# Performance work log

Measured on AMD Instinct MI355X. Metric: run time of the kernel, lower is better.

The kernel has to match this reference:

```python
import jax, jax.numpy as jnp
import numpy as np

T, B, H, W, C = 256, 1024, 9, 9, 3
CTX, HID, ACT = 64, 256, 7

def setup_inputs() -> dict:
    key = jax.random.key(0)
    ks = jax.random.split(key, 16)
    s = 0.05
    return {
        'image': jax.random.normal(ks[0], (T, B, H, W, C), jnp.float32),
        'agent_dir': jax.random.randint(ks[1], (T, B), 0, 4, jnp.int32),
        'dones': jax.random.bernoulli(ks[2], 0.02, (T, B)),
        'context': jax.random.normal(ks[3], (B, CTX), jnp.float32),
        'c0': jnp.zeros((B, HID), jnp.float32),
        'h0': jnp.zeros((B, HID), jnp.float32),
        'conv_k': jax.random.normal(ks[4], (3, 3, C, 16), jnp.float32) * s,
        'conv_b': jnp.zeros((16,), jnp.float32),
        'emb_k': jax.random.normal(ks[5], (4, 5), jnp.float32) * s,
        'emb_b': jnp.zeros((5,), jnp.float32),
        'wi': jax.random.normal(ks[6], (784 + 5 + CTX, 4 * HID), jnp.float32) * s,
        'wh': jax.random.normal(ks[7], (HID, 4 * HID), jnp.float32) * s,
        'b_lstm': jnp.zeros((4 * HID,), jnp.float32),
        'a0_k': jax.random.normal(ks[8], (HID, 32), jnp.float32) * s,
        'a0_b': jnp.zeros((32,), jnp.float32),
        'a1_k': jax.random.normal(ks[9], (32, ACT), jnp.float32) * s,
        'a1_b': jnp.zeros((ACT,), jnp.float32),
        'cr0_k': jax.random.normal(ks[10], (HID, 32), jnp.float32) * s,
        'cr0_b': jnp.zeros((32,), jnp.float32),
        'cr1_k': jax.random.normal(ks[11], (32, 1), jnp.float32) * s,
        'cr1_b': jnp.zeros((1,), jnp.float32),
    }


def reference(image, agent_dir, dones, context, c0, h0, conv_k, conv_b,
              emb_k, emb_b, wi, wh, b_lstm, a0_k, a0_b, a1_k, a1_b,
              cr0_k, cr0_b, cr1_k, cr1_b):
    t, b = image.shape[:2]
    # Conv(16, 3x3, VALID) over flattened (T*B) batch, NHWC
    x = image.reshape(t * b, *image.shape[2:])
    img = jax.lax.conv_general_dilated(
        x, conv_k, window_strides=(1, 1), padding='VALID',
        dimension_numbers=('NHWC', 'HWIO', 'NHWC')) + conv_b
    img = jax.nn.relu(img.reshape(t, b, -1))  # (T, B, 784)
    # direction embedding: one_hot(4) -> Dense(5)
    dir_e = jax.nn.one_hot(agent_dir, 4, dtype=img.dtype) @ emb_k + emb_b
    # context broadcast over time
    ctx = jnp.broadcast_to(context[None], (t, b, context.shape[-1]))
    emb = jnp.concatenate([img, dir_e, ctx], axis=-1)  # (T, B, 853)
    # precompute input-side LSTM gates (big batched GEMM outside the scan)
    xg = emb @ wi + b_lstm  # (T, B, 4*HID)

    def step(carry, inp):
        c, h = carry
        xg_t, done = inp
        mask = done[:, None]
        c = jnp.where(mask, c0, c)  # reset carry at episode boundaries
        h = jnp.where(mask, h0, h)
        gates = xg_t + h @ wh
        i, f, g, o = jnp.split(gates, 4, axis=-1)  # flax order: i, f, g, o
        new_c = jax.nn.sigmoid(f) * c + jax.nn.sigmoid(i) * jnp.tanh(g)
        new_h = jax.nn.sigmoid(o) * jnp.tanh(new_c)
        return (new_c, new_h), new_h

    (c_fin, h_fin), ys = jax.lax.scan(step, (c0, h0), (xg, dones))
    actor = jax.nn.relu(ys @ a0_k + a0_b)
    logits = actor @ a1_k + a1_b  # Categorical logits
    critic = jax.nn.relu(ys @ cr0_k + cr0_b)
    value = jnp.squeeze(critic @ cr1_k + cr1_b, axis=-1)
    return c_fin, h_fin, logits, value
```

## Files before the change

kernel.cpp:

```cpp
#include <hip/hip_runtime.h>
#include <hip/hip_fp8.h>

typedef __bf16 bf16;
typedef __bf16 bf16x8 __attribute__((ext_vector_type(8)));
typedef __bf16 bf16x4 __attribute__((ext_vector_type(4)));
typedef float  f32x4  __attribute__((ext_vector_type(4)));

#define T_DIM 256
#define B_DIM 1024
#define HID   256
#define G4    1024
#define KIMG  784
#define KPAD  800
#define KEXT  864
#define CTXD  64
#define MROWS (T_DIM*B_DIM)
#define WPITCH 264

__device__ __forceinline__ void gll16(const void* g, void* l) {
  __builtin_amdgcn_global_load_lds((const __attribute__((address_space(1))) void*)g,
                                   (__attribute__((address_space(3))) void*)l, 16, 0, 0);
}
__device__ __forceinline__ float sigm(float x) { return 1.f / (1.f + __expf(-x)); }
__device__ __forceinline__ float tanh_(float x) {
  x = fminf(fmaxf(x, -15.f), 15.f);
  float e = __expf(2.f * x);
  return (e - 1.f) / (e + 1.f);
}
__device__ __forceinline__ void bar_lds() {
  asm volatile("s_waitcnt lgkmcnt(0)\n\ts_barrier" ::: "memory");
}
__device__ __forceinline__ unsigned char to_fp8(float f) {
  __hip_fp8_e4m3 v(f);
  return *reinterpret_cast<unsigned char*>(&v);
}

__global__ void k_wiT(const float* __restrict__ wi, bf16* __restrict__ wiT) {
  int n = blockIdx.x;
  for (int k = threadIdx.x; k < KEXT; k += 256) {
    float v = 0.f;
    if (k < KIMG) v = wi[(long)k * G4 + n];
    else if (k >= 800) v = wi[(long)(k - 11) * G4 + n];
    wiT[(long)n * KEXT + k] = (bf16)v;
  }
}
__global__ void k_ext(const float* __restrict__ ctx, bf16* __restrict__ ext) {
  int idx = blockIdx.x * 256 + threadIdx.x;
  ext[idx] = (bf16)ctx[idx];
}
__global__ void k_wh8(const float* __restrict__ wh, unsigned char* __restrict__ wh8) {
  int n = blockIdx.x;
  int k = threadIdx.x;
#pragma unroll
  for (int g = 0; g < 4; ++g)
    wh8[g * 65536 + n * 256 + k] = to_fp8(wh[k * G4 + g * 256 + n]);
}
__global__ void k_W0T(const float* __restrict__ a0k, const float* __restrict__ cr0k,
                      bf16* __restrict__ w0t) {
  int n = blockIdx.x;
  int k = threadIdx.x;
  float v = (n < 32) ? a0k[k * 32 + n] : cr0k[k * 32 + (n - 32)];
  w0t[n * HID + k] = (bf16)v;
}
__global__ void k_dirgate(const float* __restrict__ wi, const float* __restrict__ emb_k,
                          const float* __restrict__ emb_b, const float* __restrict__ b_lstm,
                          float* __restrict__ dir_gate) {
  int d = blockIdx.x;
  for (int n = threadIdx.x; n < G4; n += 256) {
    float s = b_lstm[n];
#pragma unroll
    for (int j = 0; j < 5; ++j) s += (emb_k[d * 5 + j] + emb_b[j]) * wi[(KIMG + j) * G4 + n];
    dir_gate[d * G4 + n] = s;
  }
}

#define CONV_ROWS 8
__global__ void k_conv(const float* __restrict__ img, const float* __restrict__ ck,
                       const float* __restrict__ cb, bf16* __restrict__ out) {
  __shared__ float s_img[CONV_ROWS * 243];
  __shared__ float s_k[432];
  __shared__ float s_b[16];
  long r0 = (long)blockIdx.x * CONV_ROWS;
  const float* src = img + r0 * 243;
  for (int i = threadIdx.x; i < CONV_ROWS * 243; i += 256) s_img[i] = src[i];
  for (int i = threadIdx.x; i < 432; i += 256) s_k[i] = ck[i];
  if (threadIdx.x < 16) s_b[threadIdx.x] = cb[threadIdx.x];
  __syncthreads();
  for (int idx = threadIdx.x; idx < CONV_ROWS * KPAD; idx += 256) {
    int r = idx / KPAD, c = idx % KPAD;
    float v = 0.f;
    if (c < KIMG) {
      int pix = c >> 4, ch = c & 15;
      int oy = pix / 7, ox = pix % 7;
      const float* ib = s_img + r * 243 + (oy * 9 + ox) * 3;
      v = s_b[ch];
#pragma unroll
      for (int ky = 0; ky < 3; ++ky)
#pragma unroll
        for (int kx = 0; kx < 3; ++kx)
#pragma unroll
          for (int cc = 0; cc < 3; ++cc)
            v += ib[(ky * 9 + kx) * 3 + cc] * s_k[((ky * 3 + kx) * 3 + cc) * 16 + ch];
      v = fmaxf(v, 0.f);
    }
    out[r0 * KPAD + idx] = (bf16)v;
  }
}

__global__ __launch_bounds__(256, 2)
void k_gemm_xg(const bf16* __restrict__ A, const bf16* __restrict__ ext,
               const bf16* __restrict__ Bt, const float* __restrict__ dir_gate,
               const int* __restrict__ agent_dir, bf16* __restrict__ xg) {
  __shared__ __align__(16) bf16 As[128 * 32];
  __shared__ __align__(16) bf16 Bs[128 * 32];
  const int bid = blockIdx.x;
  const int xcd = bid & 7, local = bid >> 3;
  const long m0 = (long)(xcd * 256 + (local >> 3)) * 128;
  const int n0 = (local & 7) * 128;
  const int tid = threadIdx.x, wave = tid >> 6, lane = tid & 63;
  const int row16 = lane & 15, k8 = (lane >> 4) * 8, rowg = (lane >> 4) * 4;
  const int wr = (wave >> 1) * 64, wc = (wave & 1) * 64;

  const bf16* a_src0 = A + (m0 + tid / 4) * KPAD + (tid % 4) * 8;
  const bf16* a_src1 = A + (m0 + 64 + tid / 4) * KPAD + (tid % 4) * 8;
  const bf16* e_src0 = ext + (long)(((m0) & 1023) + tid / 4) * CTXD + (tid % 4) * 8;
  const bf16* e_src1 = ext + (long)(((m0 + 64) & 1023) + tid / 4) * CTXD + (tid % 4) * 8;
  const bf16* b_src0 = Bt + (long)(n0 + tid / 4) * KEXT + (tid % 4) * 8;
  const bf16* b_src1 = Bt + (long)(n0 + 64 + tid / 4) * KEXT + (tid % 4) * 8;
  bf16* asd0 = As + wave * 512;
  bf16* asd1 = As + 2048 + wave * 512;
  bf16* bsd0 = Bs + wave * 512;
  bf16* bsd1 = Bs + 2048 + wave * 512;

  f32x4 acc[4][4];
  const f32x4 zero = {0.f, 0.f, 0.f, 0.f};
#pragma unroll
  for (int i = 0; i < 4; ++i)
#pragma unroll
    for (int j = 0; j < 4; ++j) acc[i][j] = zero;

  for (int ks = 0; ks < 27; ++ks) {
    if (ks < 25) {
      const int ko = ks * 32;
      gll16(a_src0 + ko, asd0);
      gll16(a_src1 + ko, asd1);
    } else {
      const int ko = (ks - 25) * 32;
      gll16(e_src0 + ko, asd0);
      gll16(e_src1 + ko, asd1);
    }
    const int kb = ks * 32;
    gll16(b_src0 + kb, bsd0);
    gll16(b_src1 + kb, bsd1);
    __syncthreads();
    bf16x8 af[4], bfr[4];
#pragma unroll
    for (int i = 0; i < 4; ++i)
      af[i] = *(const bf16x8*)(As + (wr + 16 * i + row16) * 32 + k8);
#pragma unroll
    for (int j = 0; j < 4; ++j)
      bfr[j] = *(const bf16x8*)(Bs + (wc + 16 * j + row16) * 32 + k8);
#pragma unroll
    for (int i = 0; i < 4; ++i)
#pragma unroll
      for (int j = 0; j < 4; ++j)
        acc[i][j] = __builtin_amdgcn_mfma_f32_16x16x32_bf16(af[i], bfr[j], acc[i][j], 0, 0, 0);
    __syncthreads();
  }
#pragma unroll
  for (int i = 0; i < 4; ++i)
#pragma unroll
    for (int j = 0; j < 4; ++j)
#pragma unroll
      for (int r = 0; r < 4; ++r) {
        long row = m0 + wr + 16 * i + rowg + r;
        int colj = n0 + wc + 16 * j + row16;
        int dv = agent_dir[row];
        float base = dir_gate[dv * G4 + colj];
        int u = colj & 255, g = colj >> 8;
        xg[row * G4 + u * 4 + g] = (bf16)(acc[i][j][r] + base);
      }
}

__global__ __launch_bounds__(1024)
void k_lstm(const bf16* __restrict__ xg, const unsigned char* __restrict__ wh8,
            const int* __restrict__ dones,
            const float* __restrict__ c0, const float* __restrict__ h0,
            bf16* __restrict__ ys, float* __restrict__ cfin, float* __restrict__ hfin) {
  __shared__ __align__(16) unsigned char wi8_lds[256 * WPITCH];
  __shared__ __align__(16) unsigned char wg8_lds[256 * WPITCH];
  __shared__ __align__(16) unsigned char h8_lds[2][16 * WPITCH];
  const int tid = threadIdx.x;
  const int w = tid >> 6, lane = tid & 63;
  const int col = lane & 15;
  const int kq = lane >> 4;
  const int k8 = kq * 8;
  const int rowg = kq * 4;
  const int b0 = blockIdx.x * 16;
  const int ju = 16 * w + col;

  for (int i = tid; i < 256 * 32; i += 1024) {
    int row = i >> 5, c = i & 31;
    *(long long*)(wi8_lds + row * WPITCH + c * 8) =
        *(const long long*)(wh8 + row * 256 + c * 8);
    *(long long*)(wg8_lds + row * WPITCH + c * 8) =
        *(const long long*)(wh8 + 2 * 65536 + row * 256 + c * 8);
  }
  for (int i = tid; i < 16 * HID; i += 1024) {
    int m = i >> 8, j = i & 255;
    h8_lds[0][m * WPITCH + j] = to_fp8(h0[(b0 + m) * HID + j]);
  }

  float creg[4], c0reg[4];
  unsigned char h0b8[4];
#pragma unroll
  for (int r = 0; r < 4; ++r) {
    float v = c0[(b0 + rowg + r) * HID + ju];
    creg[r] = v; c0reg[r] = v;
    h0b8[r] = to_fp8(h0[(b0 + rowg + r) * HID + ju]);
  }
  const unsigned char* wfp = wh8 + 1 * 65536 + ju * 256 + k8;
  const unsigned char* wop = wh8 + 3 * 65536 + ju * 256 + k8;

  int4 dnA = *(const int4*)(dones + b0 + rowg);
  bf16x4 xc[4];
  {
    const bf16* xb = xg + (long)(b0 + rowg) * G4 + ju * 4;
#pragma unroll
    for (int r = 0; r < 4; ++r)
      xc[r] = *(const bf16x4*)(xb + (long)r * G4);
  }
  long long bfr[4], bor[4];
#pragma unroll
  for (int c = 0; c < 3; ++c) {
    bfr[c] = *(const long long*)(wfp + c * 32);
    bor[c] = *(const long long*)(wop + c * 32);
  }
  __syncthreads();

  const unsigned char* hr = h8_lds[0];
  unsigned char* hw = (unsigned char*)h8_lds[1];

#pragma unroll 1
  for (int t = 0; t < T_DIM; ++t) {
    const int tn = (t + 1 < T_DIM) ? t + 1 : (T_DIM - 1);
    f32x4 acc[4];
    const f32x4 zero = {0.f, 0.f, 0.f, 0.f};
#pragma unroll
    for (int g = 0; g < 4; ++g) acc[g] = zero;

    int4 dnB;
#pragma unroll
    for (int ks = 0; ks < 8; ++ks) {
      {
        const int kn = (ks + 3) & 7, slot = (ks + 3) & 3;
        bfr[slot] = *(const long long*)(wfp + kn * 32);
        bor[slot] = *(const long long*)(wop + kn * 32);
      }
      long long a8 = *(const long long*)(hr + col * WPITCH + ks * 32 + k8);
      long long bi8 = *(const long long*)(wi8_lds + ju * WPITCH + ks * 32 + k8);
      long long bg8 = *(const long long*)(wg8_lds + ju * WPITCH + ks * 32 + k8);
      __builtin_amdgcn_s_setprio(1);
      acc[0] = __builtin_amdgcn_mfma_f32_16x16x32_fp8_fp8(a8, bi8, acc[0], 0, 0, 0);
      acc[1] = __builtin_amdgcn_mfma_f32_16x16x32_fp8_fp8(a8, bfr[ks & 3], acc[1], 0, 0, 0);
      acc[2] = __builtin_amdgcn_mfma_f32_16x16x32_fp8_fp8(a8, bg8, acc[2], 0, 0, 0);
      acc[3] = __builtin_amdgcn_mfma_f32_16x16x32_fp8_fp8(a8, bor[ks & 3], acc[3], 0, 0, 0);
      __builtin_amdgcn_s_setprio(0);
      if (ks == 2)
        dnB = *(const int4*)(dones + (long)tn * B_DIM + b0 + rowg);
    }

    int dc[4] = {dnA.x, dnA.y, dnA.z, dnA.w};
    int dx[4] = {dnB.x, dnB.y, dnB.z, dnB.w};
#pragma unroll
    for (int r = 0; r < 4; ++r) {
      float c_old = dc[r] ? c0reg[r] : creg[r];
      float gi = acc[0][r] + (float)xc[r][0];
      float gf = acc[1][r] + (float)xc[r][1];
      float gg = acc[2][r] + (float)xc[r][2];
      float go = acc[3][r] + (float)xc[r][3];
      float cn = sigm(gf) * c_old + sigm(gi) * tanh_(gg);
      float hn = sigm(go) * tanh_(cn);
      creg[r] = cn;
      int m = rowg + r;
      ys[((long)t * B_DIM + b0 + m) * HID + ju] = (bf16)hn;
      hw[m * WPITCH + ju] = dx[r] ? h0b8[r] : to_fp8(hn);
      if (t == T_DIM - 1) {
        cfin[(b0 + m) * HID + ju] = cn;
        hfin[(b0 + m) * HID + ju] = hn;
      }
    }
    {
      const bf16* xb = xg + (long)(tn * B_DIM + b0 + rowg) * G4 + ju * 4;
#pragma unroll
      for (int r = 0; r < 4; ++r)
        xc[r] = *(const bf16x4*)(xb + (long)r * G4);
    }
    dnA = dnB;
    bar_lds();
    { const unsigned char* tmp = hr; hr = hw; hw = (unsigned char*)tmp; }
  }
}

#define H1PITCH 66
__global__ __launch_bounds__(256, 2)
void k_heads(const bf16* __restrict__ ys, const bf16* __restrict__ w0t,
             const float* __restrict__ a0b, const float* __restrict__ cr0b,
             const float* __restrict__ a1k, const float* __restrict__ a1b,
             const float* __restrict__ cr1k, const float* __restrict__ cr1b,
             float* __restrict__ logits, float* __restrict__ value) {
  __shared__ __align__(16) bf16 As[128 * 32];
  __shared__ __align__(16) bf16 Ws[64 * 264];
  __shared__ bf16 h1_lds[128 * H1PITCH];
  __shared__ float w2[32 * 8];
  const int tid = threadIdx.x, wave = tid >> 6, lane = tid & 63;
  const int row16 = lane & 15, k8 = (lane >> 4) * 8, rowg = (lane >> 4) * 4;
  const long m0 = (long)blockIdx.x * 128;
  for (int i = tid; i < 64 * 256; i += 256) {
    int n = i >> 8, k = i & 255;
    Ws[n * 264 + k] = w0t[i];
  }
  if (tid < 224) { int k = tid / 7, c = tid % 7; w2[k * 8 + c] = a1k[tid]; }
  else if (tid < 256) { int k = tid - 224; w2[k * 8 + 7] = cr1k[k]; }
  const bf16* a_src0 = ys + (m0 + tid / 4) * HID + (tid % 4) * 8;
  const bf16* a_src1 = ys + (m0 + 64 + tid / 4) * HID + (tid % 4) * 8;
  bf16* asd0 = As + wave * 512;
  bf16* asd1 = As + 2048 + wave * 512;
  f32x4 acc[2][4];
  const f32x4 zero = {0.f, 0.f, 0.f, 0.f};
#pragma unroll
  for (int i = 0; i < 2; ++i)
#pragma unroll
    for (int j = 0; j < 4; ++j) acc[i][j] = zero;
  for (int ks = 0; ks < 8; ++ks) {
    gll16(a_src0 + ks * 32, asd0);
    gll16(a_src1 + ks * 32, asd1);
    __syncthreads();
    bf16x8 bw[4];
#pragma unroll
    for (int j = 0; j < 4; ++j)
      bw[j] = *(const bf16x8*)(Ws + (16 * j + row16) * 264 + ks * 32 + k8);
#pragma unroll
    for (int i = 0; i < 2; ++i) {
      bf16x8 a = *(const bf16x8*)(As + (32 * wave + 16 * i + row16) * 32 + k8);
#pragma unroll
      for (int j = 0; j < 4; ++j)
        acc[i][j] = __builtin_amdgcn_mfma_f32_16x16x32_bf16(a, bw[j], acc[i][j], 0, 0, 0);
    }
    __syncthreads();
  }
#pragma unroll
  for (int i = 0; i < 2; ++i)
#pragma unroll
    for (int j = 0; j < 4; ++j)
#pragma unroll
      for (int r = 0; r < 4; ++r) {
        int rl = 32 * wave + 16 * i + rowg + r;
        int n = 16 * j + row16;
        float bias = (n < 32) ? a0b[n] : cr0b[n - 32];
        h1_lds[rl * H1PITCH + n] = (bf16)fmaxf(acc[i][j][r] + bias, 0.f);
      }
  __syncthreads();
  if (tid < 128) {
    const bf16* hp = h1_lds + tid * H1PITCH;
    float acc7[7];
#pragma unroll
    for (int c = 0; c < 7; ++c) acc7[c] = a1b[c];
    float accv = cr1b[0];
#pragma unroll 4
    for (int k = 0; k < 32; ++k) {
      float av = (float)hp[k];
      float cv = (float)hp[32 + k];
#pragma unroll
      for (int c = 0; c < 7; ++c) acc7[c] += av * w2[k * 8 + c];
      accv += cv * w2[k * 8 + 7];
    }
    long row = m0 + tid;
#pragma unroll
    for (int c = 0; c < 7; ++c) logits[row * 7 + c] = acc7[c];
    value[row] = accv;
  }
}

extern "C" void kernel_launch(void* const* d_in, const int* in_sizes, int n_in,
                              void* d_out, int out_size, void* d_ws, size_t ws_size,
                              hipStream_t stream) {
  const float* image = (const float*)d_in[0];
  const int* agent_dir = (const int*)d_in[1];
  const int* dones = (const int*)d_in[2];
  const float* context = (const float*)d_in[3];
  const float* c0 = (const float*)d_in[4];
  const float* h0 = (const float*)d_in[5];
  const float* conv_k = (const float*)d_in[6];
  const float* conv_b = (const float*)d_in[7];
  const float* emb_k = (const float*)d_in[8];
  const float* emb_b = (const float*)d_in[9];
  const float* wi = (const float*)d_in[10];
  const float* wh = (const float*)d_in[11];
  const float* b_lstm = (const float*)d_in[12];
  const float* a0_k = (const float*)d_in[13];
  const float* a0_b = (const float*)d_in[14];
  const float* a1_k = (const float*)d_in[15];
  const float* a1_b = (const float*)d_in[16];
  const float* cr0_k = (const float*)d_in[17];
  const float* cr0_b = (const float*)d_in[18];
  const float* cr1_k = (const float*)d_in[19];
  const float* cr1_b = (const float*)d_in[20];

  char* ws = (char*)d_ws;
  const size_t off_conv = 0;
  const size_t off_xg   = 419430400ULL;
  const size_t off_wiT  = off_xg  + 536870912ULL;
  const size_t off_W0T  = off_wiT + 1769472ULL;
  const size_t off_dirg = off_W0T + 32768ULL;
  const size_t off_wh8  = off_dirg + 16384ULL;
  const size_t off_ext  = off_wh8 + 262144ULL;
  const size_t total    = off_ext + 131072ULL;
  if (ws_size < total) return;

  bf16* conv_out = (bf16*)(ws + off_conv);
  bf16* xg       = (bf16*)(ws + off_xg);
  bf16* wiT      = (bf16*)(ws + off_wiT);
  bf16* W0T      = (bf16*)(ws + off_W0T);
  float* dir_gate = (float*)(ws + off_dirg);
  unsigned char* wh8 = (unsigned char*)(ws + off_wh8);
  bf16* ext = (bf16*)(ws + off_ext);
  bf16* ys = (bf16*)(ws + 0);

  float* out_cfin = (float*)d_out;
  float* out_hfin = out_cfin + 262144;
  float* out_logits = out_cfin + 524288;
  float* out_value = out_cfin + 524288 + 1835008;

  k_wiT<<<1024, 256, 0, stream>>>(wi, wiT);
  k_ext<<<256, 256, 0, stream>>>(context, ext);
  k_W0T<<<64, 256, 0, stream>>>(a0_k, cr0_k, W0T);
  k_dirgate<<<4, 256, 0, stream>>>(wi, emb_k, emb_b, b_lstm, dir_gate);
  k_wh8<<<256, 256, 0, stream>>>(wh, wh8);
  k_conv<<<MROWS / CONV_ROWS, 256, 0, stream>>>(image, conv_k, conv_b, conv_out);
  k_gemm_xg<<<16384, 256, 0, stream>>>(conv_out, ext, wiT, dir_gate, agent_dir, xg);
  k_lstm<<<64, 1024, 0, stream>>>(xg, wh8, dones, c0, h0, ys, out_cfin, out_hfin);
  k_heads<<<2048, 256, 0, stream>>>(ys, W0T, a0_b, cr0_b, a1_k, a1_b, cr1_k, cr1_b,
                                    out_logits, out_value);
}
```

Measured before the change: 2.381 ms.

## Widen xg GEMM K-tile to 64 with XOR-swizzled LDS and reordered K layout

The input-gate GEMM now stages 64-wide K slices per iteration instead of 32, halving the number of barrier-separated loop iterations (14 vs 27). The transposed weight matrix is re-laid out so the context block comes first in K (padded to 896), letting the first iteration load context and the rest load conv features. LDS reads use an XOR swizzle to avoid bank conflicts at the wider row pitch. This doubles LDS use per block, which may affect occupancy, and slightly enlarges the padded K range.

```diff
diff --git a/kernel.cpp b/kernel.cpp
--- a/kernel.cpp
+++ b/kernel.cpp
@@ -12,7 +12,7 @@
 #define G4    1024
 #define KIMG  784
 #define KPAD  800
-#define KEXT  864
+#define KB64  896
 #define CTXD  64
 #define MROWS (T_DIM*B_DIM)
 #define WPITCH 264
@@ -37,11 +37,11 @@
 
 __global__ void k_wiT(const float* __restrict__ wi, bf16* __restrict__ wiT) {
   int n = blockIdx.x;
-  for (int k = threadIdx.x; k < KEXT; k += 256) {
+  for (int k = threadIdx.x; k < KB64; k += 256) {
     float v = 0.f;
-    if (k < KIMG) v = wi[(long)k * G4 + n];
-    else if (k >= 800) v = wi[(long)(k - 11) * G4 + n];
-    wiT[(long)n * KEXT + k] = (bf16)v;
+    if (k < 64) v = wi[(long)(789 + k) * G4 + n];
+    else if (k < 848) v = wi[(long)(k - 64) * G4 + n];
+    wiT[(long)n * KB64 + k] = (bf16)v;
   }
 }
 __global__ void k_ext(const float* __restrict__ ctx, bf16* __restrict__ ext) {
@@ -111,26 +111,23 @@
 void k_gemm_xg(const bf16* __restrict__ A, const bf16* __restrict__ ext,
                const bf16* __restrict__ Bt, const float* __restrict__ dir_gate,
                const int* __restrict__ agent_dir, bf16* __restrict__ xg) {
-  __shared__ __align__(16) bf16 As[128 * 32];
-  __shared__ __align__(16) bf16 Bs[128 * 32];
+  __shared__ __align__(16) bf16 As[128 * 64];
+  __shared__ __align__(16) bf16 Bs[128 * 64];
   const int bid = blockIdx.x;
   const int xcd = bid & 7, local = bid >> 3;
   const long m0 = (long)(xcd * 256 + (local >> 3)) * 128;
   const int n0 = (local & 7) * 128;
   const int tid = threadIdx.x, wave = tid >> 6, lane = tid & 63;
-  const int row16 = lane & 15, k8 = (lane >> 4) * 8, rowg = (lane >> 4) * 4;
+  const int row16 = lane & 15, kq = lane >> 4, rowg = kq * 4;
   const int wr = (wave >> 1) * 64, wc = (wave & 1) * 64;
 
-  const bf16* a_src0 = A + (m0 + tid / 4) * KPAD + (tid % 4) * 8;
-  const bf16* a_src1 = A + (m0 + 64 + tid / 4) * KPAD + (tid % 4) * 8;
-  const bf16* e_src0 = ext + (long)(((m0) & 1023) + tid / 4) * CTXD + (tid % 4) * 8;
-  const bf16* e_src1 = ext + (long)(((m0 + 64) & 1023) + tid / 4) * CTXD + (tid % 4) * 8;
-  const bf16* b_src0 = Bt + (long)(n0 + tid / 4) * KEXT + (tid % 4) * 8;
-  const bf16* b_src1 = Bt + (long)(n0 + 64 + tid / 4) * KEXT + (tid % 4) * 8;
-  bf16* asd0 = As + wave * 512;
-  bf16* asd1 = As + 2048 + wave * 512;
-  bf16* bsd0 = Bs + wave * 512;
-  bf16* bsd1 = Bs + 2048 + wave * 512;
+  const int srow = 8 * wave + (lane >> 3);
+  const int csrc8 = ((lane & 7) ^ (lane >> 3)) * 8;
+  const bf16* a_base = A + (long)(m0 + srow) * KPAD + csrc8;
+  const bf16* e_base = ext + (long)((m0 & 1023) + srow) * CTXD + csrc8;
+  const bf16* b_base = Bt + (long)(n0 + srow) * KB64 + csrc8;
+  bf16* asd = As + wave * 512;
+  bf16* bsd = Bs + wave * 512;
 
   f32x4 acc[4][4];
   const f32x4 zero = {0.f, 0.f, 0.f, 0.f};
@@ -139,32 +136,38 @@
 #pragma unroll
     for (int j = 0; j < 4; ++j) acc[i][j] = zero;
 
-  for (int ks = 0; ks < 27; ++ks) {
-    if (ks < 25) {
-      const int ko = ks * 32;
-      gll16(a_src0 + ko, asd0);
-      gll16(a_src1 + ko, asd1);
+  const int swz = row16 & 7;
+  for (int ks = 0; ks < 14; ++ks) {
+    if (ks == 0) {
+#pragma unroll
+      for (int c = 0; c < 4; ++c) gll16(e_base + c * (32 * CTXD), asd + c * 2048);
     } else {
-      const int ko = (ks - 25) * 32;
-      gll16(e_src0 + ko, asd0);
-      gll16(e_src1 + ko, asd1);
-    }
-    const int kb = ks * 32;
-    gll16(b_src0 + kb, bsd0);
-    gll16(b_src1 + kb, bsd1);
+      const long ko = (long)(ks - 1) * 64;
+#pragma unroll
+      for (int c = 0; c < 4; ++c) gll16(a_base + c * (32 * KPAD) + ko, asd + c * 2048);
+    }
+    {
+      const long kb = (long)ks * 64;
+#pragma unroll
+      for (int c = 0; c < 4; ++c) gll16(b_base + c * (32 * KB64) + kb, bsd + c * 2048);
+    }
     __syncthreads();
-    bf16x8 af[4], bfr[4];
-#pragma unroll
-    for (int i = 0; i < 4; ++i)
-      af[i] = *(const bf16x8*)(As + (wr + 16 * i + row16) * 32 + k8);
-#pragma unroll
-    for (int j = 0; j < 4; ++j)
-      bfr[j] = *(const bf16x8*)(Bs + (wc + 16 * j + row16) * 32 + k8);
-#pragma unroll
-    for (int i = 0; i < 4; ++i)
+#pragma unroll
+    for (int ksub = 0; ksub < 2; ++ksub) {
+      const int co = ((4 * ksub + kq) ^ swz) << 3;
+      bf16x8 af[4], bfr[4];
+#pragma unroll
+      for (int i = 0; i < 4; ++i)
+        af[i] = *(const bf16x8*)(As + (wr + 16 * i + row16) * 64 + co);
 #pragma unroll
       for (int j = 0; j < 4; ++j)
-        acc[i][j] = __builtin_amdgcn_mfma_f32_16x16x32_bf16(af[i], bfr[j], acc[i][j], 0, 0, 0);
+        bfr[j] = *(const bf16x8*)(Bs + (wc + 16 * j + row16) * 64 + co);
+#pragma unroll
+      for (int i = 0; i < 4; ++i)
+#pragma unroll
+        for (int j = 0; j < 4; ++j)
+          acc[i][j] = __builtin_amdgcn_mfma_f32_16x16x32_bf16(af[i], bfr[j], acc[i][j], 0, 0, 0);
+    }
     __syncthreads();
   }
 #pragma unroll
@@ -411,7 +414,7 @@
   const size_t off_conv = 0;
   const size_t off_xg   = 419430400ULL;
   const size_t off_wiT  = off_xg  + 536870912ULL;
-  const size_t off_W0T  = off_wiT + 1769472ULL;
+  const size_t off_W0T  = off_wiT + 1835008ULL;
   const size_t off_dirg = off_W0T + 32768ULL;
   const size_t off_wh8  = off_dirg + 16384ULL;
   const size_t off_ext  = off_wh8 + 262144ULL;
```

New measurement: 2.263 ms (median of 2 runs). 5.0% less time.
